# Kernel tuning notes

Measured on AMD Instinct MI355X. Metric: run time of the kernel, lower is better.

Reference implementation:

```python
import jax, jax.numpy as jnp
import numpy as np

B, D, H, W = 32, 256, 32, 32
K = 2048


def setup_inputs() -> dict:
    key = jax.random.key(0)
    k1, k2 = jax.random.split(key)
    x = jax.random.normal(k1, (B, D, H, W), dtype=jnp.float32)
    # nn.Parameter uniform_(-0.5, 0.5), shape [embedding_dim, num_embeddings]
    embedding_table = jax.random.uniform(k2, (D, K), dtype=jnp.float32, minval=-0.5, maxval=0.5)
    return {"x": x, "embedding_table": embedding_table}


def _l2norm(v, axis):
    return v / jnp.maximum(jnp.linalg.norm(v, axis=axis, keepdims=True), 1e-12)


def reference(x, embedding_table):
    b, d, h, w = x.shape
    k = embedding_table.shape[1]
    # [B,C,H,W] -> [B,H,W,C] -> [N,D]
    flat_x = jnp.transpose(x, (0, 2, 3, 1)).reshape(-1, d)

    # l2-normalized vectors used only for distance computation
    fx = _l2norm(flat_x, axis=1)
    et = _l2norm(embedding_table, axis=0)

    # ||fx||^2 - 2 fx.et + ||et||^2  -> [N,K]
    distances = (
        jnp.sum(fx * fx, axis=1, keepdims=True)
        - 2.0 * (fx @ et)
        + jnp.sum(et * et, axis=0, keepdims=True)
    )
    encoding_indices = jnp.argmin(distances, axis=1)  # [N]

    # gather from UNnormalized table (matches original), -> [B,H,W,D] -> [B,D,H,W]
    quantized = embedding_table.T[encoding_indices].reshape(b, h, w, d)
    quantized_x = jnp.transpose(quantized, (0, 3, 1, 2))

    dictionary_loss = jnp.mean((jax.lax.stop_gradient(x) - quantized_x) ** 2)
    commitment_loss = jnp.mean((x - jax.lax.stop_gradient(quantized_x)) ** 2)

    # straight-through estimator
    quantized_x = x + jax.lax.stop_gradient(quantized_x - x)

    counts = jnp.bincount(encoding_indices, length=k)
    probs = counts / jnp.sum(counts)
    entropy_loss = jnp.sum(probs * jnp.log(probs + 1e-10))

    return (
        quantized_x,
        dictionary_loss,
        commitment_loss,
        entropy_loss,
        encoding_indices.reshape(b, -1),
    )
```

## Files before the change

### kernel.cpp

```cpp
#include <hip/hip_runtime.h>
#include <hip/hip_bf16.h>
#include <hip/hip_fp16.h>
#include <math.h>

#define KN 2048
#define DN 256
#define NN 32768
#define HW 1024
#define XSTR 260

typedef _Float16 half8 __attribute__((ext_vector_type(8)));
typedef float floatx4 __attribute__((ext_vector_type(4)));


__global__ __launch_bounds__(256) void k_norm(const float* __restrict__ E,
                                              double* __restrict__ norminv) {
  const int c = blockIdx.x * 256 + threadIdx.x;
  const float* p = E + c;
  double s = 0.0;
#pragma unroll 8
  for (int d = 0; d < DN; ++d) {
    double v = (double)p[(size_t)d * KN];
    s = fma(v, v, s);
  }
  double nr = sqrt(s);
  if (nr < 1e-12) nr = 1e-12;
  norminv[c] = 1.0 / nr;
}

__global__ __launch_bounds__(256) void k_convE(const float* __restrict__ E,
                                               const double* __restrict__ norminv,
                                               _Float16* __restrict__ Et) {
  const int c = ((blockIdx.x & 7) << 8) + threadIdx.x;
  const int dg = blockIdx.x >> 3;
  const int kh = dg >> 2, lg = dg & 3;
  const int nc = c >> 7, w = (c >> 5) & 3, nf = (c >> 4) & 1, col16 = c & 15;
  const int t = nc * 8 + kh;
  const double inv = norminv[c];
  const size_t base =
      (size_t)t * 8192 + w * 2048 + nf * 512 + (lg * 16 + col16) * 8;
  half8 hv, lv;
#pragma unroll
  for (int j = 0; j < 8; ++j) {
    float v = (float)((double)E[(size_t)(dg * 8 + j) * KN + c] * inv);
    _Float16 h = (_Float16)v;
    hv[j] = h;
    lv[j] = (_Float16)((v - (float)h) * 4096.0f);
  }
  *(half8*)(Et + base) = hv;
  *(half8*)(Et + base + 1024) = lv;
}

__device__ __forceinline__ void gload_lds16(const void* g, void* l) {
  __builtin_amdgcn_global_load_lds(
      (const __attribute__((address_space(1))) unsigned int*)g,
      (__attribute__((address_space(3))) unsigned int*)l, 16, 0, 0);
}

#define STAGE(t, buf)                                                        \
  {                                                                          \
    const size_t gb_ = (size_t)(t) * 8192;                                   \
    const int lb_ = (buf) * 16384;                                           \
    _Pragma("unroll") for (int q_ = 0; q_ < 4; ++q_)                         \
        gload_lds16(Et + gb_ + q_ * 2048 + tid * 8,                          \
                    lds + lb_ + q_ * 4096 + tid * 16);                       \
  }

#define ITER(nc, kh, WAITOP, DO_STAGE)                                       \
  {                                                                          \
    asm volatile(WAITOP ::: "memory");                                       \
    __builtin_amdgcn_s_barrier();                                            \
    __builtin_amdgcn_sched_barrier(0);                                       \
    const int t_ = (nc)*8 + (kh);                                            \
    if (DO_STAGE) { STAGE(t_ + 3, (t_ + 3) & 3); }                           \
    const char* wb_ = lds + (t_ & 3) * 16384 + w * 4096;                     \
    half8 bh_[2], bl_[2];                                                    \
    bh_[0] = *(const half8*)(wb_ + lane * 16);                               \
    bh_[1] = *(const half8*)(wb_ + 1024 + lane * 16);                        \
    bl_[0] = *(const half8*)(wb_ + 2048 + lane * 16);                        \
    bl_[1] = *(const half8*)(wb_ + 3072 + lane * 16);                        \
    __builtin_amdgcn_s_setprio(1);                                           \
    _Pragma("unroll") for (int mf_ = 0; mf_ < 2; ++mf_)                      \
        _Pragma("unroll") for (int nf_ = 0; nf_ < 2; ++nf_) {                \
      accm[mf_][nf_] = __builtin_amdgcn_mfma_f32_16x16x32_f16(               \
          ah[mf_][(kh)], bh_[nf_], accm[mf_][nf_], 0, 0, 0);                 \
      accc[mf_][nf_] = __builtin_amdgcn_mfma_f32_16x16x32_f16(               \
          ah[mf_][(kh)], bl_[nf_], accc[mf_][nf_], 0, 0, 0);                 \
      accc[mf_][nf_] = __builtin_amdgcn_mfma_f32_16x16x32_f16(               \
          al[mf_][(kh)], bh_[nf_], accc[mf_][nf_], 0, 0, 0);                 \
    }                                                                        \
    __builtin_amdgcn_s_setprio(0);                                           \
  }

#define ZEROACC                                                              \
  {                                                                          \
    _Pragma("unroll") for (int mf_ = 0; mf_ < 2; ++mf_)                      \
        _Pragma("unroll") for (int nf_ = 0; nf_ < 2; ++nf_) {                \
      accm[mf_][nf_] = (floatx4)0.0f;                                        \
      accc[mf_][nf_] = (floatx4)0.0f;                                        \
    }                                                                        \
  }

#define EPILOGUE(nc)                                                         \
  {                                                                          \
    _Pragma("unroll") for (int nf_ = 0; nf_ < 2; ++nf_) {                    \
      const int c_ = (nc)*128 + w * 32 + nf_ * 16 + c16;                     \
      _Pragma("unroll") for (int mf_ = 0; mf_ < 2; ++mf_)                    \
          _Pragma("unroll") for (int r_ = 0; r_ < 4; ++r_) {                 \
        const double s_ = (double)accm[mf_][nf_][r_] +                       \
                          (double)accc[mf_][nf_][r_] * (1.0 / 4096.0);       \
        if (s_ > best[mf_][r_]) { best[mf_][r_] = s_; bidx[mf_][r_] = c_; }  \
      }                                                                      \
    }                                                                        \
  }

#define W8 "s_waitcnt vmcnt(8)"
#define W4 "s_waitcnt vmcnt(4)"
#define W0 "s_waitcnt vmcnt(0)"

__global__ __launch_bounds__(256, 2) void k_score(
    const float* __restrict__ x, const _Float16* __restrict__ Et,
    int* __restrict__ idx_ws, float* __restrict__ fidx_out,
    int* __restrict__ counts) {
  __shared__ __align__(16) char lds[65536];
  const int tid = threadIdx.x;
  const int lane = tid & 63;
  const int w = tid >> 6;
  const int lg = lane >> 4;
  const int c16 = lane & 15;
  const int rowbase = blockIdx.x * 32;

  {
    float* xs = (float*)lds;
    const int r = tid & 31;
    const int d0 = tid >> 5;
    const int n = rowbase + r;
    const float* xb = x + (size_t)(n >> 10) * (DN * HW) + (n & 1023);
#pragma unroll
    for (int d = d0; d < DN; d += 8)
      xs[r * XSTR + d] = xb[(size_t)d * HW];
  }
  __syncthreads();

  half8 ah[2][8], al[2][8];
  {
    const float* xs = (const float*)lds;
#pragma unroll
    for (int mf = 0; mf < 2; ++mf)
#pragma unroll
      for (int kh = 0; kh < 8; ++kh) {
        const float* p = xs + (mf * 16 + c16) * XSTR + kh * 32 + lg * 8;
        half8 h, l;
#pragma unroll
        for (int i = 0; i < 8; ++i) {
          float v = p[i];
          _Float16 hh = (_Float16)v;
          h[i] = hh;
          l[i] = (_Float16)((v - (float)hh) * 4096.0f);
        }
        ah[mf][kh] = h;
        al[mf][kh] = l;
      }
  }
  __syncthreads();

  double best[2][4];
  int bidx[2][4];
#pragma unroll
  for (int mf = 0; mf < 2; ++mf)
#pragma unroll
    for (int r = 0; r < 4; ++r) { best[mf][r] = -1e300; bidx[mf][r] = 0; }

  floatx4 accm[2][2], accc[2][2];

  STAGE(0, 0);
  STAGE(1, 1);
  STAGE(2, 2);

  for (int nc = 0; nc < 15; ++nc) {
    ZEROACC;
    ITER(nc, 0, W8, 1);
    ITER(nc, 1, W8, 1);
    ITER(nc, 2, W8, 1);
    ITER(nc, 3, W8, 1);
    ITER(nc, 4, W8, 1);
    ITER(nc, 5, W8, 1);
    ITER(nc, 6, W8, 1);
    ITER(nc, 7, W8, 1);
    EPILOGUE(nc);
  }
  ZEROACC;
  ITER(15, 0, W8, 1);
  ITER(15, 1, W8, 1);
  ITER(15, 2, W8, 1);
  ITER(15, 3, W8, 1);
  ITER(15, 4, W8, 1);
  ITER(15, 5, W8, 0);
  ITER(15, 6, W4, 0);
  ITER(15, 7, W0, 0);
  EPILOGUE(15);

  __syncthreads();
  double* redD = (double*)lds;
  int* redI = (int*)(lds + 16384);
  const int ent = w * 16 + c16;
#pragma unroll
  for (int mf = 0; mf < 2; ++mf)
#pragma unroll
    for (int r = 0; r < 4; ++r) {
      const int row = mf * 16 + lg * 4 + r;
      redD[row * 64 + ent] = best[mf][r];
      redI[row * 64 + ent] = bidx[mf][r];
    }
  __syncthreads();
  if (tid < 32) {
    double bd = -1e300;
    int bi = 1 << 30;
    for (int e = 0; e < 64; ++e) {
      double dv = redD[tid * 64 + e];
      int iv = redI[tid * 64 + e];
      if (dv > bd || (dv == bd && iv < bi)) { bd = dv; bi = iv; }
    }
    const int n = rowbase + tid;
    idx_ws[n] = bi;
    fidx_out[n] = (float)bi;
    atomicAdd(&counts[bi], 1);
  }
}

__global__ __launch_bounds__(256) void k_quant(const float* __restrict__ x,
                                               const float* __restrict__ E,
                                               const int* __restrict__ idx,
                                               float* __restrict__ out,
                                               float* __restrict__ lossparts) {
  const int T = blockIdx.x * 256 + threadIdx.x;
  const int w4 = T & 7;
  int rest = T >> 3;
  const int h = rest & 31;
  rest >>= 5;
  const int d = rest & 255;
  const int b = rest >> 8;
  const int n = b * 1024 + h * 32 + w4 * 4;
  const int4 iv = *(const int4*)(idx + n);
  const size_t xoff = ((size_t)(b * 256 + d) << 10) + h * 32 + w4 * 4;
  const float4 xv = *(const float4*)(x + xoff);
  const float* Er = E + (size_t)d * KN;
  float4 q;
  q.x = Er[iv.x];
  q.y = Er[iv.y];
  q.z = Er[iv.z];
  q.w = Er[iv.w];
  *(float4*)(out + xoff) = q;
  const float dx = xv.x - q.x, dy = xv.y - q.y, dz = xv.z - q.z, dw = xv.w - q.w;
  float s = dx * dx + dy * dy + dz * dz + dw * dw;
#pragma unroll
  for (int off = 32; off > 0; off >>= 1) s += __shfl_down(s, off, 64);
  __shared__ float red[4];
  const int lane = threadIdx.x & 63, wv = threadIdx.x >> 6;
  if (lane == 0) red[wv] = s;
  __syncthreads();
  if (threadIdx.x == 0)
    atomicAdd(&lossparts[blockIdx.x & 255], red[0] + red[1] + red[2] + red[3]);
}

__global__ __launch_bounds__(256) void k_final(const int* __restrict__ counts,
                                               const float* __restrict__ lossparts,
                                               float* __restrict__ out) {
  __shared__ double redE[256];
  __shared__ double redL[256];
  const int tid = threadIdx.x;
  double t = 0.0;
  for (int u = tid; u < KN; u += 256) {
    float p = (float)counts[u] * (1.0f / 32768.0f);
    t += (double)(p * logf(p + 1e-10f));
  }
  redE[tid] = t;
  redL[tid] = (double)lossparts[tid];
  __syncthreads();
  for (int s2 = 128; s2 > 0; s2 >>= 1) {
    if (tid < s2) {
      redE[tid] += redE[tid + s2];
      redL[tid] += redL[tid + s2];
    }
    __syncthreads();
  }
  if (tid == 0) {
    float L = (float)(redL[0] * (1.0 / 8388608.0));
    out[8388608] = L;
    out[8388609] = L;
    out[8388610] = (float)redE[0];
  }
}

extern "C" void kernel_launch(void* const* d_in, const int* in_sizes, int n_in,
                              void* d_out, int out_size, void* d_ws, size_t ws_size,
                              hipStream_t stream) {
  const float* x = (const float*)d_in[0];
  const float* E = (const float*)d_in[1];
  float* out = (float*)d_out;
  char* ws = (char*)d_ws;
  int* counts = (int*)ws;
  float* lossparts = (float*)(ws + 8192);
  double* norminv = (double*)(ws + 16384);
  int* idx = (int*)(ws + 32768);
  _Float16* Et = (_Float16*)(ws + 163840);

  hipMemsetAsync(ws, 0, 9216, stream);
  k_norm<<<8, 256, 0, stream>>>(E, norminv);
  k_convE<<<256, 256, 0, stream>>>(E, norminv, Et);
  k_score<<<NN / 32, 256, 0, stream>>>(x, Et, idx, out + 8388611, counts);
  k_quant<<<(NN * DN / 4) / 256, 256, 0, stream>>>(x, E, idx, out, lossparts);
  k_final<<<1, 256, 0, stream>>>(counts, lossparts, out);
}
```

Baseline: 232.1 us.

## Cut score LDS ring to three stages, split norm kernel, fuse final reduction

The score kernel's Et staging ring shrinks from four 16KB buffers to three (48KB LDS). Prefetch distance drops from 3 to 2 tiles, and the launch bound goes from 2 to 3 blocks per CU to raise occupancy. The column-norm kernel now spreads over 64 blocks, each accumulating a partial sum of squares with double atomics, and the sqrt/reciprocal moves into the conversion kernel. The final entropy/loss kernel is folded into the quant kernel through a last-block-done counter, which removes one launch. The risks are less latency hiding from the shallower prefetch, register pressure at 3 blocks per CU, and atomic contention.

```diff
diff --git a/kernel.cpp b/kernel.cpp
--- a/kernel.cpp
+++ b/kernel.cpp
@@ -14,29 +14,30 @@
 
 
 __global__ __launch_bounds__(256) void k_norm(const float* __restrict__ E,
-                                              double* __restrict__ norminv) {
-  const int c = blockIdx.x * 256 + threadIdx.x;
-  const float* p = E + c;
+                                              double* __restrict__ normsq) {
+  const int c = ((blockIdx.x & 7) << 8) + threadIdx.x;
+  const int ds = blockIdx.x >> 3;
+  const float* p = E + (size_t)(ds * 32) * KN + c;
   double s = 0.0;
 #pragma unroll 8
-  for (int d = 0; d < DN; ++d) {
+  for (int d = 0; d < 32; ++d) {
     double v = (double)p[(size_t)d * KN];
     s = fma(v, v, s);
   }
-  double nr = sqrt(s);
-  if (nr < 1e-12) nr = 1e-12;
-  norminv[c] = 1.0 / nr;
+  atomicAdd(&normsq[c], s);
 }
 
 __global__ __launch_bounds__(256) void k_convE(const float* __restrict__ E,
-                                               const double* __restrict__ norminv,
+                                               const double* __restrict__ normsq,
                                                _Float16* __restrict__ Et) {
   const int c = ((blockIdx.x & 7) << 8) + threadIdx.x;
   const int dg = blockIdx.x >> 3;
   const int kh = dg >> 2, lg = dg & 3;
   const int nc = c >> 7, w = (c >> 5) & 3, nf = (c >> 4) & 1, col16 = c & 15;
   const int t = nc * 8 + kh;
-  const double inv = norminv[c];
+  double nr = sqrt(normsq[c]);
+  if (nr < 1e-12) nr = 1e-12;
+  const double inv = 1.0 / nr;
   const size_t base =
       (size_t)t * 8192 + w * 2048 + nf * 512 + (lg * 16 + col16) * 8;
   half8 hv, lv;
@@ -66,14 +67,14 @@
                     lds + lb_ + q_ * 4096 + tid * 16);                       \
   }
 
-#define ITER(nc, kh, WAITOP, DO_STAGE)                                       \
+#define ITER(nc, ncp, kh, WAITOP, DO_STAGE)                                  \
   {                                                                          \
     asm volatile(WAITOP ::: "memory");                                       \
     __builtin_amdgcn_s_barrier();                                            \
     __builtin_amdgcn_sched_barrier(0);                                       \
     const int t_ = (nc)*8 + (kh);                                            \
-    if (DO_STAGE) { STAGE(t_ + 3, (t_ + 3) & 3); }                           \
-    const char* wb_ = lds + (t_ & 3) * 16384 + w * 4096;                     \
+    if (DO_STAGE) { STAGE(t_ + 2, ((2 * (ncp) + (kh) + 2) % 3)); }           \
+    const char* wb_ = lds + ((2 * (ncp) + (kh)) % 3) * 16384 + w * 4096;     \
     half8 bh_[2], bl_[2];                                                    \
     bh_[0] = *(const half8*)(wb_ + lane * 16);                               \
     bh_[1] = *(const half8*)(wb_ + 1024 + lane * 16);                        \
@@ -114,15 +115,14 @@
     }                                                                        \
   }
 
-#define W8 "s_waitcnt vmcnt(8)"
 #define W4 "s_waitcnt vmcnt(4)"
 #define W0 "s_waitcnt vmcnt(0)"
 
-__global__ __launch_bounds__(256, 2) void k_score(
+__global__ __launch_bounds__(256, 3) void k_score(
     const float* __restrict__ x, const _Float16* __restrict__ Et,
     int* __restrict__ idx_ws, float* __restrict__ fidx_out,
     int* __restrict__ counts) {
-  __shared__ __align__(16) char lds[65536];
+  __shared__ __align__(16) char lds[49152];
   const int tid = threadIdx.x;
   const int lane = tid & 63;
   const int w = tid >> 6;
@@ -175,29 +175,32 @@
 
   STAGE(0, 0);
   STAGE(1, 1);
-  STAGE(2, 2);
-
-  for (int nc = 0; nc < 15; ++nc) {
-    ZEROACC;
-    ITER(nc, 0, W8, 1);
-    ITER(nc, 1, W8, 1);
-    ITER(nc, 2, W8, 1);
-    ITER(nc, 3, W8, 1);
-    ITER(nc, 4, W8, 1);
-    ITER(nc, 5, W8, 1);
-    ITER(nc, 6, W8, 1);
-    ITER(nc, 7, W8, 1);
-    EPILOGUE(nc);
+
+  for (int nc3 = 0; nc3 < 5; ++nc3) {
+#pragma unroll
+    for (int ncp = 0; ncp < 3; ++ncp) {
+      const int nc = nc3 * 3 + ncp;
+      ZEROACC;
+      ITER(nc, ncp, 0, W4, 1);
+      ITER(nc, ncp, 1, W4, 1);
+      ITER(nc, ncp, 2, W4, 1);
+      ITER(nc, ncp, 3, W4, 1);
+      ITER(nc, ncp, 4, W4, 1);
+      ITER(nc, ncp, 5, W4, 1);
+      ITER(nc, ncp, 6, W4, 1);
+      ITER(nc, ncp, 7, W4, 1);
+      EPILOGUE(nc);
+    }
   }
   ZEROACC;
-  ITER(15, 0, W8, 1);
-  ITER(15, 1, W8, 1);
-  ITER(15, 2, W8, 1);
-  ITER(15, 3, W8, 1);
-  ITER(15, 4, W8, 1);
-  ITER(15, 5, W8, 0);
-  ITER(15, 6, W4, 0);
-  ITER(15, 7, W0, 0);
+  ITER(15, 0, 0, W4, 1);
+  ITER(15, 0, 1, W4, 1);
+  ITER(15, 0, 2, W4, 1);
+  ITER(15, 0, 3, W4, 1);
+  ITER(15, 0, 4, W4, 1);
+  ITER(15, 0, 5, W4, 1);
+  ITER(15, 0, 6, W4, 0);
+  ITER(15, 0, 7, W0, 0);
   EPILOGUE(15);
 
   __syncthreads();
@@ -232,7 +235,9 @@
                                                const float* __restrict__ E,
                                                const int* __restrict__ idx,
                                                float* __restrict__ out,
-                                               float* __restrict__ lossparts) {
+                                               float* __restrict__ lossparts,
+                                               const int* __restrict__ counts,
+                                               int* __restrict__ donecnt) {
   const int T = blockIdx.x * 256 + threadIdx.x;
   const int w4 = T & 7;
   int rest = T >> 3;
@@ -256,26 +261,29 @@
 #pragma unroll
   for (int off = 32; off > 0; off >>= 1) s += __shfl_down(s, off, 64);
   __shared__ float red[4];
-  const int lane = threadIdx.x & 63, wv = threadIdx.x >> 6;
+  const int tid = threadIdx.x;
+  const int lane = tid & 63, wv = tid >> 6;
   if (lane == 0) red[wv] = s;
   __syncthreads();
-  if (threadIdx.x == 0)
+  __shared__ int lastFlag;
+  if (tid == 0) {
     atomicAdd(&lossparts[blockIdx.x & 255], red[0] + red[1] + red[2] + red[3]);
-}
-
-__global__ __launch_bounds__(256) void k_final(const int* __restrict__ counts,
-                                               const float* __restrict__ lossparts,
-                                               float* __restrict__ out) {
+    __threadfence();
+    lastFlag = (atomicAdd(donecnt, 1) == 8191);
+  }
+  __syncthreads();
+  if (!lastFlag) return;
+  __threadfence();
+
   __shared__ double redE[256];
   __shared__ double redL[256];
-  const int tid = threadIdx.x;
   double t = 0.0;
   for (int u = tid; u < KN; u += 256) {
     float p = (float)counts[u] * (1.0f / 32768.0f);
     t += (double)(p * logf(p + 1e-10f));
   }
   redE[tid] = t;
-  redL[tid] = (double)lossparts[tid];
+  redL[tid] = (double)atomicAdd(&lossparts[tid], 0.0f);
   __syncthreads();
   for (int s2 = 128; s2 > 0; s2 >>= 1) {
     if (tid < s2) {
@@ -301,14 +309,15 @@
   char* ws = (char*)d_ws;
   int* counts = (int*)ws;
   float* lossparts = (float*)(ws + 8192);
-  double* norminv = (double*)(ws + 16384);
+  int* donecnt = (int*)(ws + 9216);
+  double* normsq = (double*)(ws + 16384);
   int* idx = (int*)(ws + 32768);
   _Float16* Et = (_Float16*)(ws + 163840);
 
-  hipMemsetAsync(ws, 0, 9216, stream);
-  k_norm<<<8, 256, 0, stream>>>(E, norminv);
-  k_convE<<<256, 256, 0, stream>>>(E, norminv, Et);
+  hipMemsetAsync(ws, 0, 32768, stream);
+  k_norm<<<64, 256, 0, stream>>>(E, normsq);
+  k_convE<<<256, 256, 0, stream>>>(E, normsq, Et);
   k_score<<<NN / 32, 256, 0, stream>>>(x, Et, idx, out + 8388611, counts);
-  k_quant<<<(NN * DN / 4) / 256, 256, 0, stream>>>(x, E, idx, out, lossparts);
-  k_final<<<1, 256, 0, stream>>>(counts, lossparts, out);
-}
+  k_quant<<<(NN * DN / 4) / 256, 256, 0, stream>>>(x, E, idx, out, lossparts,
+                                                   counts, donecnt);
+}
```

Result: slower. 682.1 us (+193.9%).
